# Performance work log

Hardware: AMD Instinct MI355X
Metric: run time of the kernel (lower is better)

Reference implementation:

```python
import jax, jax.numpy as jnp
import numpy as np

D, K = 512, 32


def setup_inputs() -> dict:
    key = jax.random.key(0)
    k1, k2, k3 = jax.random.split(key, 3)
    X = jax.random.normal(k1, (8, D, 128, 128), dtype=jnp.float32)
    std1 = 1.0 / (K * D) ** 0.5
    codewords = jax.random.uniform(k2, (K, D), dtype=jnp.float32, minval=-std1, maxval=std1)
    scale = jax.random.uniform(k3, (K,), dtype=jnp.float32, minval=-1.0, maxval=0.0)
    return {"X": X, "codewords": codewords, "scale": scale}


def reference(X, codewords, scale):
    B = X.shape[0]
    # [B, D, H, W] -> [B, N, D]
    Xf = X.reshape(B, D, -1).transpose(0, 2, 1)
    # scaled L2: s_k * ||x_i - d_k||^2, expanded to avoid [B,N,K,D] residuals
    x2 = jnp.sum(Xf * Xf, axis=-1, keepdims=True)            # [B, N, 1]
    c2 = jnp.sum(codewords * codewords, axis=-1)              # [K]
    xc = jnp.einsum('bnd,kd->bnk', Xf, codewords)             # [B, N, K]
    sl = scale * (x2 - 2.0 * xc + c2)                         # [B, N, K]
    A = jax.nn.softmax(sl, axis=2)                            # [B, N, K]
    # E[b,k,d] = sum_n A[b,n,k] * (X[b,n,d] - C[k,d])
    E = jnp.einsum('bnk,bnd->bkd', A, Xf) - jnp.sum(A, axis=1)[..., None] * codewords
    return E
```

## Files before the change

kernel.cpp:

```cpp
#include <hip/hip_runtime.h>
#include <stdint.h>

#define B_ 8
#define D_ 512
#define N_ 16384
#define K_ 32

typedef __attribute__((ext_vector_type(8))) short short8;
typedef __attribute__((ext_vector_type(16))) float f32x16;

union F8 { short8 v; unsigned short s[8]; uint32_t u[4]; uint4 q; };

__device__ __forceinline__ uint32_t bfpack2(float lo, float hi) {
    uint32_t a = __float_as_uint(lo);
    uint32_t b = __float_as_uint(hi);
    a += 0x7FFFu + ((a >> 16) & 1u);
    b += 0x7FFFu + ((b >> 16) & 1u);
    return (a >> 16) | (b & 0xFFFF0000u);
}

__device__ __forceinline__ void bar_lds() {
    __builtin_amdgcn_sched_barrier(0);
    __builtin_amdgcn_s_waitcnt(0xC07F);
    __builtin_amdgcn_s_barrier();
    __builtin_amdgcn_sched_barrier(0);
}

__launch_bounds__(256, 2)
__global__ void encode_kernel(const float* __restrict__ X,
                              const float* __restrict__ Cg,
                              const float* __restrict__ scale,
                              float* __restrict__ part,
                              float* __restrict__ aSumAcc)
{
    __shared__ uint32_t xsTw[D_ * 20];
    __shared__ float    lgp[4][32][36];
    __shared__ uint32_t A_ldsw[K_ * 20];
    __shared__ float    x2p[4][32];
    __shared__ float    scs[K_], c2s[K_];
    __shared__ float    c2tmp[K_][9];
    __shared__ float    aSumLds[K_];

    unsigned short* xsTs  = (unsigned short*)xsTw;
    unsigned short* A_lds = (unsigned short*)A_ldsw;

    const int tid = threadIdx.x;
    const int l   = tid & 63;
    const int w   = __builtin_amdgcn_readfirstlane(tid >> 6);
    const int lc  = l & 31;
    const int nh  = l >> 5;
    const int b     = blockIdx.x >> 6;
    const int chunk = blockIdx.x & 63;

    {
        int k = tid >> 3, dg = tid & 7;
        const float* cr = Cg + k * D_ + dg * 64;
        float s2 = 0.f;
#pragma unroll
        for (int i = 0; i < 16; ++i) {
            float4 v = *(const float4*)(cr + i * 4);
            s2 += v.x * v.x + v.y * v.y + v.z * v.z + v.w * v.w;
        }
        c2tmp[k][dg] = s2;
        if (tid < K_) { scs[tid] = scale[tid]; aSumLds[tid] = 0.f; }
    }
    __syncthreads();
    if (tid < K_) {
        float s = 0.f;
#pragma unroll
        for (int dg = 0; dg < 8; ++dg) s += c2tmp[tid][dg];
        c2s[tid] = s;
    }

    F8 cfr[8];
#pragma unroll
    for (int ss = 0; ss < 8; ++ss) {
        int d0 = (8 * w + ss) * 16 + nh * 8;
        const float* cp = Cg + lc * D_ + d0;
        float4 a  = *(const float4*)(cp);
        float4 bq = *(const float4*)(cp + 4);
        cfr[ss].u[0] = bfpack2(a.x, a.y);
        cfr[ss].u[1] = bfpack2(a.z, a.w);
        cfr[ss].u[2] = bfpack2(bq.x, bq.y);
        cfr[ss].u[3] = bfpack2(bq.z, bq.w);
    }

    f32x16 eacc[4];
#pragma unroll
    for (int ti = 0; ti < 4; ++ti)
#pragma unroll
        for (int r = 0; r < 16; ++r) eacc[ti][r] = 0.f;
    float aSumReg[4] = {0.f, 0.f, 0.f, 0.f};

    const int nl  = l >> 3;
    const int kq  = l & 7;
    const int smn = w * 8 + nl;
    const int k0  = kq * 4;

    const int o  = tid >> 3;
    const int nq = tid & 7;
    const size_t xbase = (size_t)b * D_ * N_ + (size_t)chunk * 256;

    float4 pf[16];
    {
        const float* Xp = X + xbase + nq * 4;
#pragma unroll
        for (int r = 0; r < 16; ++r)
            pf[r] = *(const float4*)(Xp + (size_t)(o + 32 * r) * N_);
    }

    for (int t = 0; t < 8; ++t) {
        bar_lds();

        {
            float4 x2a; x2a.x = x2a.y = x2a.z = x2a.w = 0.f;
#pragma unroll
            for (int r = 0; r < 16; ++r) {
                int d = o + 32 * r;
                float4 v = pf[r];
                x2a.x += v.x * v.x; x2a.y += v.y * v.y;
                x2a.z += v.z * v.z; x2a.w += v.w * v.w;
                uint2 p;
                p.x = bfpack2(v.x, v.y);
                p.y = bfpack2(v.z, v.w);
                *(uint2*)&xsTw[d * 20 + nq * 2] = p;
            }
#pragma unroll
            for (int m = 8; m <= 32; m <<= 1) {
                x2a.x += __shfl_xor(x2a.x, m);
                x2a.y += __shfl_xor(x2a.y, m);
                x2a.z += __shfl_xor(x2a.z, m);
                x2a.w += __shfl_xor(x2a.w, m);
            }
            if (l < 8) *(float4*)&x2p[w][nq * 4] = x2a;
        }

        {
            int tn = (t < 7) ? t + 1 : 7;
            const float* Xp = X + xbase + tn * 32 + nq * 4;
#pragma unroll
            for (int r = 0; r < 16; ++r)
                pf[r] = *(const float4*)(Xp + (size_t)(o + 32 * r) * N_);
        }

        bar_lds();

        f32x16 lacc;
#pragma unroll
        for (int r = 0; r < 16; ++r) lacc[r] = 0.f;
#pragma unroll
        for (int ss = 0; ss < 8; ++ss) {
            int d0 = (8 * w + ss) * 16 + nh * 8;
            F8 af;
#pragma unroll
            for (int j = 0; j < 8; ++j)
                af.s[j] = xsTs[(d0 + j) * 40 + lc];
            lacc = __builtin_amdgcn_mfma_f32_32x32x16_bf16(af.v, cfr[ss].v, lacc, 0, 0, 0);
        }
#pragma unroll
        for (int r = 0; r < 16; ++r)
            lgp[w][(r & 3) + 8 * (r >> 2) + 4 * nh][lc] = lacc[r];

        bar_lds();

        {
            float4 xc = *(const float4*)&lgp[0][smn][k0];
            float4 x1 = *(const float4*)&lgp[1][smn][k0];
            float4 x2q = *(const float4*)&lgp[2][smn][k0];
            float4 x3 = *(const float4*)&lgp[3][smn][k0];
            xc.x += x1.x + x2q.x + x3.x;
            xc.y += x1.y + x2q.y + x3.y;
            xc.z += x1.z + x2q.z + x3.z;
            xc.w += x1.w + x2q.w + x3.w;
            float x2v = x2p[0][smn] + x2p[1][smn] + x2p[2][smn] + x2p[3][smn];
            float sl0 = scs[k0]     * (x2v - 2.f * xc.x + c2s[k0]);
            float sl1 = scs[k0 + 1] * (x2v - 2.f * xc.y + c2s[k0 + 1]);
            float sl2 = scs[k0 + 2] * (x2v - 2.f * xc.z + c2s[k0 + 2]);
            float sl3 = scs[k0 + 3] * (x2v - 2.f * xc.w + c2s[k0 + 3]);
            float m = fmaxf(fmaxf(sl0, sl1), fmaxf(sl2, sl3));
#pragma unroll
            for (int mk = 1; mk <= 4; mk <<= 1) m = fmaxf(m, __shfl_xor(m, mk));
            float e0 = __expf(sl0 - m), e1 = __expf(sl1 - m);
            float e2 = __expf(sl2 - m), e3 = __expf(sl3 - m);
            float s = e0 + e1 + e2 + e3;
#pragma unroll
            for (int mk = 1; mk <= 4; mk <<= 1) s += __shfl_xor(s, mk);
            float inv = 1.f / s;
            e0 *= inv; e1 *= inv; e2 *= inv; e3 *= inv;
            aSumReg[0] += e0; aSumReg[1] += e1;
            aSumReg[2] += e2; aSumReg[3] += e3;
            A_lds[(k0)     * 40 + smn] = (unsigned short)(bfpack2(e0, 0.f));
            A_lds[(k0 + 1) * 40 + smn] = (unsigned short)(bfpack2(e1, 0.f));
            A_lds[(k0 + 2) * 40 + smn] = (unsigned short)(bfpack2(e2, 0.f));
            A_lds[(k0 + 3) * 40 + smn] = (unsigned short)(bfpack2(e3, 0.f));
        }

        bar_lds();

#pragma unroll
        for (int ti = 0; ti < 4; ++ti) {
            int dcol = (4 * w + ti) * 32 + lc;
#pragma unroll
            for (int ns = 0; ns < 2; ++ns) {
                F8 af, bf;
                af.q = *(const uint4*)&A_lds[lc * 40 + ns * 16 + nh * 8];
                bf.q = *(const uint4*)&xsTs[dcol * 40 + ns * 16 + nh * 8];
                eacc[ti] = __builtin_amdgcn_mfma_f32_32x32x16_bf16(af.v, bf.v, eacc[ti], 0, 0, 0);
            }
        }
    }

    float* pB = part + (size_t)blockIdx.x * (K_ * D_);
#pragma unroll
    for (int ti = 0; ti < 4; ++ti) {
        int d = (4 * w + ti) * 32 + lc;
#pragma unroll
        for (int r = 0; r < 16; ++r) {
            int k = (r & 3) + 8 * (r >> 2) + 4 * nh;
            pB[k * D_ + d] = eacc[ti][r];
        }
    }

#pragma unroll
    for (int i = 0; i < 4; ++i) {
#pragma unroll
        for (int m = 8; m <= 32; m <<= 1) aSumReg[i] += __shfl_xor(aSumReg[i], m);
    }
    if (l < 8) {
#pragma unroll
        for (int i = 0; i < 4; ++i) unsafeAtomicAdd(&aSumLds[k0 + i], aSumReg[i]);
    }
    __syncthreads();
    if (tid < K_) unsafeAtomicAdd(&aSumAcc[b * K_ + tid], aSumLds[tid]);
}

__global__ void finish_kernel(const float* __restrict__ part,
                              const float* __restrict__ aSumAcc,
                              const float* __restrict__ Cg,
                              float* __restrict__ out)
{
    int idx = blockIdx.x * 256 + threadIdx.x;
    int kd = idx & (K_ * D_ - 1);
    int b  = idx >> 14;
    int k  = kd >> 9;
    const float* p = part + (size_t)b * 64 * (K_ * D_) + kd;
    float s = 0.f;
#pragma unroll 8
    for (int c = 0; c < 64; ++c) s += p[(size_t)c * (K_ * D_)];
    out[idx] = s - aSumAcc[(b << 5) + k] * Cg[kd];
}

extern "C" void kernel_launch(void* const* d_in, const int* in_sizes, int n_in,
                              void* d_out, int out_size, void* d_ws, size_t ws_size,
                              hipStream_t stream)
{
    const float* X  = (const float*)d_in[0];
    const float* C  = (const float*)d_in[1];
    const float* sc = (const float*)d_in[2];
    float* out = (float*)d_out;

    float* part    = (float*)d_ws;
    float* aSumAcc = part + (size_t)512 * K_ * D_;

    hipMemsetAsync(aSumAcc, 0, B_ * K_ * sizeof(float), stream);
    encode_kernel<<<B_ * 64, 256, 0, stream>>>(X, C, sc, part, aSumAcc);
    finish_kernel<<<(B_ * K_ * D_) / 256, 256, 0, stream>>>(part, aSumAcc, C, out);
}
```

Before: 385.9 us.

## Split encode work across 8 waves, drop register prefetch, store logits as bf16

The encode kernel goes from 256 to 512 threads per block, so each wave handles half the D range in both MFMA stages. The register-held prefetch of the next X tile is removed: X is loaded directly each iteration, and latency hiding now relies on more resident waves instead of software pipelining. Per-wave partial logits are written to LDS as bf16 rather than fp32, which adds rounding error to the distance computation. The sched_barrier fences are also dropped, and only half the waves run the softmax step.

```diff
diff --git a/kernel.cpp b/kernel.cpp
--- a/kernel.cpp
+++ b/kernel.cpp
@@ -18,15 +18,20 @@
     b += 0x7FFFu + ((b >> 16) & 1u);
     return (a >> 16) | (b & 0xFFFF0000u);
 }
+__device__ __forceinline__ unsigned short bf16of(float x) {
+    uint32_t a = __float_as_uint(x);
+    a += 0x7FFFu + ((a >> 16) & 1u);
+    return (unsigned short)(a >> 16);
+}
+__device__ __forceinline__ float bflo(uint32_t v) { return __uint_as_float(v << 16); }
+__device__ __forceinline__ float bfhi(uint32_t v) { return __uint_as_float(v & 0xFFFF0000u); }
 
 __device__ __forceinline__ void bar_lds() {
-    __builtin_amdgcn_sched_barrier(0);
     __builtin_amdgcn_s_waitcnt(0xC07F);
     __builtin_amdgcn_s_barrier();
-    __builtin_amdgcn_sched_barrier(0);
-}
-
-__launch_bounds__(256, 2)
+}
+
+__launch_bounds__(512, 4)
 __global__ void encode_kernel(const float* __restrict__ X,
                               const float* __restrict__ Cg,
                               const float* __restrict__ scale,
@@ -34,11 +39,11 @@
                               float* __restrict__ aSumAcc)
 {
     __shared__ uint32_t xsTw[D_ * 20];
-    __shared__ float    lgp[4][32][36];
+    __shared__ unsigned short lgpS[8 * 32 * 40];
     __shared__ uint32_t A_ldsw[K_ * 20];
-    __shared__ float    x2p[4][32];
+    __shared__ float    x2p[8][32];
     __shared__ float    scs[K_], c2s[K_];
-    __shared__ float    c2tmp[K_][9];
+    __shared__ float    c2tmp[K_][17];
     __shared__ float    aSumLds[K_];
 
     unsigned short* xsTs  = (unsigned short*)xsTw;
@@ -53,11 +58,11 @@
     const int chunk = blockIdx.x & 63;
 
     {
-        int k = tid >> 3, dg = tid & 7;
-        const float* cr = Cg + k * D_ + dg * 64;
+        int k = tid >> 4, dg = tid & 15;
+        const float* cr = Cg + k * D_ + dg * 32;
         float s2 = 0.f;
 #pragma unroll
-        for (int i = 0; i < 16; ++i) {
+        for (int i = 0; i < 8; ++i) {
             float4 v = *(const float4*)(cr + i * 4);
             s2 += v.x * v.x + v.y * v.y + v.z * v.z + v.w * v.w;
         }
@@ -68,14 +73,14 @@
     if (tid < K_) {
         float s = 0.f;
 #pragma unroll
-        for (int dg = 0; dg < 8; ++dg) s += c2tmp[tid][dg];
+        for (int dg = 0; dg < 16; ++dg) s += c2tmp[tid][dg];
         c2s[tid] = s;
     }
 
-    F8 cfr[8];
-#pragma unroll
-    for (int ss = 0; ss < 8; ++ss) {
-        int d0 = (8 * w + ss) * 16 + nh * 8;
+    F8 cfr[4];
+#pragma unroll
+    for (int ss = 0; ss < 4; ++ss) {
+        int d0 = 64 * w + ss * 16 + nh * 8;
         const float* cp = Cg + lc * D_ + d0;
         float4 a  = *(const float4*)(cp);
         float4 bq = *(const float4*)(cp + 4);
@@ -85,39 +90,32 @@
         cfr[ss].u[3] = bfpack2(bq.z, bq.w);
     }
 
-    f32x16 eacc[4];
-#pragma unroll
-    for (int ti = 0; ti < 4; ++ti)
+    f32x16 eacc[2];
+#pragma unroll
+    for (int ti = 0; ti < 2; ++ti)
 #pragma unroll
         for (int r = 0; r < 16; ++r) eacc[ti][r] = 0.f;
     float aSumReg[4] = {0.f, 0.f, 0.f, 0.f};
 
     const int nl  = l >> 3;
     const int kq  = l & 7;
-    const int smn = w * 8 + nl;
+    const int smn = (w & 3) * 8 + nl;
     const int k0  = kq * 4;
 
-    const int o  = tid >> 3;
+    const int dl = tid >> 3;
     const int nq = tid & 7;
     const size_t xbase = (size_t)b * D_ * N_ + (size_t)chunk * 256;
 
-    float4 pf[16];
-    {
-        const float* Xp = X + xbase + nq * 4;
-#pragma unroll
-        for (int r = 0; r < 16; ++r)
-            pf[r] = *(const float4*)(Xp + (size_t)(o + 32 * r) * N_);
-    }
-
     for (int t = 0; t < 8; ++t) {
         bar_lds();
 
         {
+            const float* Xp = X + xbase + t * 32 + nq * 4;
             float4 x2a; x2a.x = x2a.y = x2a.z = x2a.w = 0.f;
 #pragma unroll
-            for (int r = 0; r < 16; ++r) {
-                int d = o + 32 * r;
-                float4 v = pf[r];
+            for (int r = 0; r < 8; ++r) {
+                int d = dl + 64 * r;
+                float4 v = *(const float4*)(Xp + (size_t)d * N_);
                 x2a.x += v.x * v.x; x2a.y += v.y * v.y;
                 x2a.z += v.z * v.z; x2a.w += v.w * v.w;
                 uint2 p;
@@ -135,48 +133,45 @@
             if (l < 8) *(float4*)&x2p[w][nq * 4] = x2a;
         }
 
+        bar_lds();
+
         {
-            int tn = (t < 7) ? t + 1 : 7;
-            const float* Xp = X + xbase + tn * 32 + nq * 4;
-#pragma unroll
-            for (int r = 0; r < 16; ++r)
-                pf[r] = *(const float4*)(Xp + (size_t)(o + 32 * r) * N_);
-        }
-
-        bar_lds();
-
-        f32x16 lacc;
-#pragma unroll
-        for (int r = 0; r < 16; ++r) lacc[r] = 0.f;
-#pragma unroll
-        for (int ss = 0; ss < 8; ++ss) {
-            int d0 = (8 * w + ss) * 16 + nh * 8;
-            F8 af;
-#pragma unroll
-            for (int j = 0; j < 8; ++j)
-                af.s[j] = xsTs[(d0 + j) * 40 + lc];
-            lacc = __builtin_amdgcn_mfma_f32_32x32x16_bf16(af.v, cfr[ss].v, lacc, 0, 0, 0);
-        }
-#pragma unroll
-        for (int r = 0; r < 16; ++r)
-            lgp[w][(r & 3) + 8 * (r >> 2) + 4 * nh][lc] = lacc[r];
-
-        bar_lds();
-
-        {
-            float4 xc = *(const float4*)&lgp[0][smn][k0];
-            float4 x1 = *(const float4*)&lgp[1][smn][k0];
-            float4 x2q = *(const float4*)&lgp[2][smn][k0];
-            float4 x3 = *(const float4*)&lgp[3][smn][k0];
-            xc.x += x1.x + x2q.x + x3.x;
-            xc.y += x1.y + x2q.y + x3.y;
-            xc.z += x1.z + x2q.z + x3.z;
-            xc.w += x1.w + x2q.w + x3.w;
-            float x2v = x2p[0][smn] + x2p[1][smn] + x2p[2][smn] + x2p[3][smn];
-            float sl0 = scs[k0]     * (x2v - 2.f * xc.x + c2s[k0]);
-            float sl1 = scs[k0 + 1] * (x2v - 2.f * xc.y + c2s[k0 + 1]);
-            float sl2 = scs[k0 + 2] * (x2v - 2.f * xc.z + c2s[k0 + 2]);
-            float sl3 = scs[k0 + 3] * (x2v - 2.f * xc.w + c2s[k0 + 3]);
+            f32x16 lacc;
+#pragma unroll
+            for (int r = 0; r < 16; ++r) lacc[r] = 0.f;
+#pragma unroll
+            for (int ss = 0; ss < 4; ++ss) {
+                int d0 = 64 * w + ss * 16 + nh * 8;
+                F8 af;
+#pragma unroll
+                for (int j = 0; j < 8; ++j)
+                    af.s[j] = xsTs[(d0 + j) * 40 + lc];
+                lacc = __builtin_amdgcn_mfma_f32_32x32x16_bf16(af.v, cfr[ss].v, lacc, 0, 0, 0);
+            }
+#pragma unroll
+            for (int r = 0; r < 16; ++r) {
+                int row = (r & 3) + 8 * (r >> 2) + 4 * nh;
+                lgpS[(w * 32 + row) * 40 + lc] = bf16of(lacc[r]);
+            }
+        }
+
+        bar_lds();
+
+        if (w < 4) {
+            float xc0 = 0.f, xc1 = 0.f, xc2 = 0.f, xc3 = 0.f;
+#pragma unroll
+            for (int wp = 0; wp < 8; ++wp) {
+                uint2 pv = *(const uint2*)&lgpS[(wp * 32 + smn) * 40 + k0];
+                xc0 += bflo(pv.x); xc1 += bfhi(pv.x);
+                xc2 += bflo(pv.y); xc3 += bfhi(pv.y);
+            }
+            float x2v = 0.f;
+#pragma unroll
+            for (int wp = 0; wp < 8; ++wp) x2v += x2p[wp][smn];
+            float sl0 = scs[k0]     * (x2v - 2.f * xc0 + c2s[k0]);
+            float sl1 = scs[k0 + 1] * (x2v - 2.f * xc1 + c2s[k0 + 1]);
+            float sl2 = scs[k0 + 2] * (x2v - 2.f * xc2 + c2s[k0 + 2]);
+            float sl3 = scs[k0 + 3] * (x2v - 2.f * xc3 + c2s[k0 + 3]);
             float m = fmaxf(fmaxf(sl0, sl1), fmaxf(sl2, sl3));
 #pragma unroll
             for (int mk = 1; mk <= 4; mk <<= 1) m = fmaxf(m, __shfl_xor(m, mk));
@@ -189,17 +184,17 @@
             e0 *= inv; e1 *= inv; e2 *= inv; e3 *= inv;
             aSumReg[0] += e0; aSumReg[1] += e1;
             aSumReg[2] += e2; aSumReg[3] += e3;
-            A_lds[(k0)     * 40 + smn] = (unsigned short)(bfpack2(e0, 0.f));
-            A_lds[(k0 + 1) * 40 + smn] = (unsigned short)(bfpack2(e1, 0.f));
-            A_lds[(k0 + 2) * 40 + smn] = (unsigned short)(bfpack2(e2, 0.f));
-            A_lds[(k0 + 3) * 40 + smn] = (unsigned short)(bfpack2(e3, 0.f));
-        }
-
-        bar_lds();
-
-#pragma unroll
-        for (int ti = 0; ti < 4; ++ti) {
-            int dcol = (4 * w + ti) * 32 + lc;
+            A_lds[(k0)     * 40 + smn] = bf16of(e0);
+            A_lds[(k0 + 1) * 40 + smn] = bf16of(e1);
+            A_lds[(k0 + 2) * 40 + smn] = bf16of(e2);
+            A_lds[(k0 + 3) * 40 + smn] = bf16of(e3);
+        }
+
+        bar_lds();
+
+#pragma unroll
+        for (int ti = 0; ti < 2; ++ti) {
+            int dcol = 64 * w + 32 * ti + lc;
 #pragma unroll
             for (int ns = 0; ns < 2; ++ns) {
                 F8 af, bf;
@@ -212,8 +207,8 @@
 
     float* pB = part + (size_t)blockIdx.x * (K_ * D_);
 #pragma unroll
-    for (int ti = 0; ti < 4; ++ti) {
-        int d = (4 * w + ti) * 32 + lc;
+    for (int ti = 0; ti < 2; ++ti) {
+        int d = 64 * w + 32 * ti + lc;
 #pragma unroll
         for (int r = 0; r < 16; ++r) {
             int k = (r & 3) + 8 * (r >> 2) + 4 * nh;
@@ -221,14 +216,16 @@
         }
     }
 
-#pragma unroll
-    for (int i = 0; i < 4; ++i) {
-#pragma unroll
-        for (int m = 8; m <= 32; m <<= 1) aSumReg[i] += __shfl_xor(aSumReg[i], m);
-    }
-    if (l < 8) {
-#pragma unroll
-        for (int i = 0; i < 4; ++i) unsafeAtomicAdd(&aSumLds[k0 + i], aSumReg[i]);
+    if (w < 4) {
+#pragma unroll
+        for (int i = 0; i < 4; ++i) {
+#pragma unroll
+            for (int m = 8; m <= 32; m <<= 1) aSumReg[i] += __shfl_xor(aSumReg[i], m);
+        }
+        if (l < 8) {
+#pragma unroll
+            for (int i = 0; i < 4; ++i) unsafeAtomicAdd(&aSumLds[k0 + i], aSumReg[i]);
+        }
     }
     __syncthreads();
     if (tid < K_) unsafeAtomicAdd(&aSumAcc[b * K_ + tid], aSumLds[tid]);
@@ -263,6 +260,6 @@
     float* aSumAcc = part + (size_t)512 * K_ * D_;
 
     hipMemsetAsync(aSumAcc, 0, B_ * K_ * sizeof(float), stream);
-    encode_kernel<<<B_ * 64, 256, 0, stream>>>(X, C, sc, part, aSumAcc);
+    encode_kernel<<<B_ * 64, 512, 0, stream>>>(X, C, sc, part, aSumAcc);
     finish_kernel<<<(B_ * K_ * D_) / 256, 256, 0, stream>>>(part, aSumAcc, C, out);
 }
```

Result: no change. 385.2 us (-0.2%).
